# Optimization experiments

Measured on AMD Instinct MI355X. Metric: run time of the kernel, lower is better.

The kernel has to match this reference:

```python
import jax, jax.numpy as jnp
import numpy as np

N, E, D = 10000, 160000, 512


def setup_inputs() -> dict:
    key = jax.random.key(0)
    ks = jax.random.split(key, 5)
    x = jax.random.normal(ks[0], (N, D), dtype=jnp.float32)
    edge_index = jax.random.randint(ks[1], (2, E), 0, N, dtype=jnp.int32)
    W = jax.random.normal(ks[2], (D, D), dtype=jnp.float32) * (1.0 / np.sqrt(D))
    a_src = jax.random.normal(ks[3], (D,), dtype=jnp.float32) * 0.1
    a_dst = jax.random.normal(ks[4], (D,), dtype=jnp.float32) * 0.1
    bias = jnp.zeros((D,), dtype=jnp.float32)
    return {"x": x, "edge_index": edge_index, "W": W,
            "a_src": a_src, "a_dst": a_dst, "bias": bias}


def reference(x, edge_index, W, a_src, a_dst, bias):
    n = x.shape[0]
    # PyG GATConv default: add self-loops
    loops = jnp.arange(n, dtype=edge_index.dtype)
    src = jnp.concatenate([edge_index[0], loops])  # [E+N]
    dst = jnp.concatenate([edge_index[1], loops])  # [E+N]

    h = x @ W.T                                    # [N, D] linear projection
    e_src = h @ a_src                              # [N]
    e_dst = h @ a_dst                              # [N]
    e = e_src[src] + e_dst[dst]                    # [E+N]
    neg_slope = 0.2
    e = jnp.where(e > 0, e, neg_slope * e)         # leaky_relu

    # per-destination softmax (stable); self-loops guarantee non-empty segments
    m = jax.ops.segment_max(e, dst, num_segments=n)
    e = jnp.exp(e - m[dst])
    s = jax.ops.segment_sum(e, dst, num_segments=n)
    alpha = e / s[dst]                             # [E+N]

    msg = alpha[:, None] * h[src]                  # [E+N, D]
    out = jax.ops.segment_sum(msg, dst, num_segments=n) + bias  # [N, D]

    # module forward: x + elu(gat(x, edge_index))
    return x + jax.nn.elu(out)
```

## Files before the change

kernel.cpp:

```cpp
#include <hip/hip_runtime.h>
#include <hip/hip_bf16.h>

using bf16x8 = __attribute__((ext_vector_type(8))) __bf16;
using f32x4  = __attribute__((ext_vector_type(4))) float;
typedef unsigned int u32;

#define DFEAT 512
#define SLOTS 64

static __device__ __forceinline__ unsigned short f2bfbits(float f) {
    union { float f; unsigned int u; } v; v.f = f;
    unsigned int u = v.u;
    unsigned int r = (u + 0x7fffu + ((u >> 16) & 1u)) >> 16;
    return (unsigned short)r;
}

static __device__ __forceinline__ void gload16(const unsigned short* g, unsigned short* l) {
    __builtin_amdgcn_global_load_lds(
        (const __attribute__((address_space(1))) u32*)g,
        (__attribute__((address_space(3))) u32*)l, 16, 0, 0);
}

__global__ __launch_bounds__(256) void cvt_scatter_kernel(
    const float* __restrict__ x, const float* __restrict__ w,
    unsigned short* __restrict__ Xb, unsigned short* __restrict__ Wb,
    const int* __restrict__ srcv, const int* __restrict__ dstv,
    int* __restrict__ cur, int* __restrict__ slot,
    int nx4, int ntot4, int E, int T)
{
    int i = blockIdx.x * 256 + threadIdx.x;
    if (i < ntot4) {
        const float* in = (i < nx4) ? x : w;
        unsigned short* o = (i < nx4) ? Xb : Wb;
        int j = (i < nx4) ? i : i - nx4;
        float4 v = ((const float4*)in)[j];
        ushort4 u;
        u.x = f2bfbits(v.x); u.y = f2bfbits(v.y);
        u.z = f2bfbits(v.z); u.w = f2bfbits(v.w);
        ((ushort4*)o)[j] = u;
    }
    if (i < T) {
        int s, d;
        if (i < E) { s = srcv[i]; d = dstv[i]; }
        else       { s = d = i - E; }
        int pos = atomicAdd(&cur[d], 1);
        if (pos < SLOTS) slot[(size_t)d * SLOTS + pos] = s;
    }
}

__global__ __launch_bounds__(256, 5) void gemm_h_kernel(
    const unsigned short* __restrict__ X, const unsigned short* __restrict__ Wm,
    const float* __restrict__ avs, const float* __restrict__ avd,
    unsigned short* __restrict__ H, float* __restrict__ es, float* __restrict__ ed,
    int N)
{
    __shared__ unsigned short Asm[2][64 * 64];
    __shared__ unsigned short Bsm[2][64 * 64];

    int L = blockIdx.x;
    int xcd = L & 7;
    int q   = L >> 3;
    int rpan = (q >> 3) * 8 + xcd;
    int cpan = q & 7;
    int rowPanels = (N + 63) >> 6;
    if (rpan >= rowPanels) return;
    int bm = rpan * 64;
    int bn = cpan * 64;

    int tid  = threadIdx.x;
    int wave = tid >> 6;
    int lane = tid & 63;
    int l15  = lane & 15;
    int quad = lane >> 4;

    int srow   = lane >> 3;
    int schunk = (lane & 7) ^ (srow & 7);
    int arow0 = bm + wave * 16 + srow;
    int arow1 = arow0 + 8;
    arow0 = arow0 < N ? arow0 : N - 1;
    arow1 = arow1 < N ? arow1 : N - 1;
    const unsigned short* gA0 = X  + (size_t)arow0 * DFEAT + schunk * 8;
    const unsigned short* gA1 = X  + (size_t)arow1 * DFEAT + schunk * 8;
    const unsigned short* gB0 = Wm + (size_t)(bn + wave * 16 + srow) * DFEAT + schunk * 8;
    const unsigned short* gB1 = gB0 + (size_t)8 * DFEAT;

    auto stage = [&](int buf, int s) {
        int ko = s * 64;
        gload16(gA0 + ko, &Asm[buf][(wave * 16 + 0) * 64]);
        gload16(gA1 + ko, &Asm[buf][(wave * 16 + 8) * 64]);
        gload16(gB0 + ko, &Bsm[buf][(wave * 16 + 0) * 64]);
        gload16(gB1 + ko, &Bsm[buf][(wave * 16 + 8) * 64]);
    };

    f32x4 acc[4] = {};
    int xa = l15 & 7;
    int aoff = (wave * 16 + l15) * 128;

    auto compute = [&](int buf) {
        const char* Ab = (const char*)&Asm[buf][0];
        const char* Bb = (const char*)&Bsm[buf][0];
        #pragma unroll
        for (int ks = 0; ks < 2; ++ks) {
            int cb = ((ks * 4 + quad) ^ xa) * 16;
            bf16x8 a  = *(const bf16x8*)(Ab + aoff + cb);
            bf16x8 b0 = *(const bf16x8*)(Bb + (0 * 16 + l15) * 128 + cb);
            bf16x8 b1 = *(const bf16x8*)(Bb + (1 * 16 + l15) * 128 + cb);
            bf16x8 b2 = *(const bf16x8*)(Bb + (2 * 16 + l15) * 128 + cb);
            bf16x8 b3 = *(const bf16x8*)(Bb + (3 * 16 + l15) * 128 + cb);
            acc[0] = __builtin_amdgcn_mfma_f32_16x16x32_bf16(a, b0, acc[0], 0, 0, 0);
            acc[1] = __builtin_amdgcn_mfma_f32_16x16x32_bf16(a, b1, acc[1], 0, 0, 0);
            acc[2] = __builtin_amdgcn_mfma_f32_16x16x32_bf16(a, b2, acc[2], 0, 0, 0);
            acc[3] = __builtin_amdgcn_mfma_f32_16x16x32_bf16(a, b3, acc[3], 0, 0, 0);
        }
    };

    stage(0, 0);
    __syncthreads();
    int buf = 0;
    for (int s = 0; s < 7; ++s) {
        stage(buf ^ 1, s + 1);
        compute(buf);
        __syncthreads();
        buf ^= 1;
    }
    compute(buf);

    float as[4], ad[4];
    #pragma unroll
    for (int nt = 0; nt < 4; ++nt) {
        as[nt] = avs[bn + nt * 16 + l15];
        ad[nt] = avd[bn + nt * 16 + l15];
    }

    int rbase = bm + wave * 16 + quad * 4;
    #pragma unroll
    for (int nt = 0; nt < 4; ++nt) {
        int col = bn + nt * 16 + l15;
        #pragma unroll
        for (int r = 0; r < 4; ++r) {
            int row = rbase + r;
            if (row < N) H[(size_t)row * DFEAT + col] = f2bfbits(acc[nt][r]);
        }
    }
    #pragma unroll
    for (int r = 0; r < 4; ++r) {
        float ps = acc[0][r] * as[0] + acc[1][r] * as[1]
                 + acc[2][r] * as[2] + acc[3][r] * as[3];
        float pd = acc[0][r] * ad[0] + acc[1][r] * ad[1]
                 + acc[2][r] * ad[2] + acc[3][r] * ad[3];
        #pragma unroll
        for (int m = 1; m < 16; m <<= 1) {
            ps += __shfl_xor(ps, m);
            pd += __shfl_xor(pd, m);
        }
        int row = rbase + r;
        if (l15 == 0 && row < N) {
            atomicAdd(&es[row], ps);
            atomicAdd(&ed[row], pd);
        }
    }
}

__global__ __launch_bounds__(256) void aggregate_kernel(
    const unsigned short* __restrict__ H, const float* __restrict__ x,
    const float* __restrict__ bias,
    const int* __restrict__ cur, const int* __restrict__ slot,
    const float* __restrict__ es, const float* __restrict__ ed,
    float* __restrict__ out, int N)
{
    int node = (blockIdx.x * 256 + threadIdx.x) >> 6;
    int lane = threadIdx.x & 63;
    if (node >= N) return;

    int k = cur[node];
    if (k > SLOTS) k = SLOTS;

    int   s = 0;
    float w = 0.f;
    if (lane < k) {
        s = slot[(size_t)node * SLOTS + lane];
        float e = es[s] + ed[node];
        e = e > 0.f ? e : 0.2f * e;
        w = __expf(e);
    }
    float denom = w;
    #pragma unroll
    for (int off = 32; off > 0; off >>= 1) denom += __shfl_xor(denom, off);
    float inv = 1.0f / denom;

    float a[8] = {};
    const unsigned short* Hl = H + lane * 8;

    auto accum = [&](int sj, float wj) {
        uint4 hv = *(const uint4*)(Hl + (size_t)sj * DFEAT);
        a[0] += wj * __uint_as_float(hv.x << 16);
        a[1] += wj * __uint_as_float(hv.x & 0xffff0000u);
        a[2] += wj * __uint_as_float(hv.y << 16);
        a[3] += wj * __uint_as_float(hv.y & 0xffff0000u);
        a[4] += wj * __uint_as_float(hv.z << 16);
        a[5] += wj * __uint_as_float(hv.z & 0xffff0000u);
        a[6] += wj * __uint_as_float(hv.w << 16);
        a[7] += wj * __uint_as_float(hv.w & 0xffff0000u);
    };

    int j = 0;
    for (; j + 3 < k; j += 4) {
        int   s0 = __shfl(s, j),     s1 = __shfl(s, j + 1);
        int   s2 = __shfl(s, j + 2), s3 = __shfl(s, j + 3);
        float w0 = __shfl(w, j),     w1 = __shfl(w, j + 1);
        float w2 = __shfl(w, j + 2), w3 = __shfl(w, j + 3);
        uint4 h0 = *(const uint4*)(Hl + (size_t)s0 * DFEAT);
        uint4 h1 = *(const uint4*)(Hl + (size_t)s1 * DFEAT);
        uint4 h2 = *(const uint4*)(Hl + (size_t)s2 * DFEAT);
        uint4 h3 = *(const uint4*)(Hl + (size_t)s3 * DFEAT);
        a[0] += w0 * __uint_as_float(h0.x << 16);
        a[1] += w0 * __uint_as_float(h0.x & 0xffff0000u);
        a[2] += w0 * __uint_as_float(h0.y << 16);
        a[3] += w0 * __uint_as_float(h0.y & 0xffff0000u);
        a[4] += w0 * __uint_as_float(h0.z << 16);
        a[5] += w0 * __uint_as_float(h0.z & 0xffff0000u);
        a[6] += w0 * __uint_as_float(h0.w << 16);
        a[7] += w0 * __uint_as_float(h0.w & 0xffff0000u);
        a[0] += w1 * __uint_as_float(h1.x << 16);
        a[1] += w1 * __uint_as_float(h1.x & 0xffff0000u);
        a[2] += w1 * __uint_as_float(h1.y << 16);
        a[3] += w1 * __uint_as_float(h1.y & 0xffff0000u);
        a[4] += w1 * __uint_as_float(h1.z << 16);
        a[5] += w1 * __uint_as_float(h1.z & 0xffff0000u);
        a[6] += w1 * __uint_as_float(h1.w << 16);
        a[7] += w1 * __uint_as_float(h1.w & 0xffff0000u);
        a[0] += w2 * __uint_as_float(h2.x << 16);
        a[1] += w2 * __uint_as_float(h2.x & 0xffff0000u);
        a[2] += w2 * __uint_as_float(h2.y << 16);
        a[3] += w2 * __uint_as_float(h2.y & 0xffff0000u);
        a[4] += w2 * __uint_as_float(h2.z << 16);
        a[5] += w2 * __uint_as_float(h2.z & 0xffff0000u);
        a[6] += w2 * __uint_as_float(h2.w << 16);
        a[7] += w2 * __uint_as_float(h2.w & 0xffff0000u);
        a[0] += w3 * __uint_as_float(h3.x << 16);
        a[1] += w3 * __uint_as_float(h3.x & 0xffff0000u);
        a[2] += w3 * __uint_as_float(h3.y << 16);
        a[3] += w3 * __uint_as_float(h3.y & 0xffff0000u);
        a[4] += w3 * __uint_as_float(h3.z << 16);
        a[5] += w3 * __uint_as_float(h3.z & 0xffff0000u);
        a[6] += w3 * __uint_as_float(h3.w << 16);
        a[7] += w3 * __uint_as_float(h3.w & 0xffff0000u);
    }
    for (; j < k; ++j) accum(__shfl(s, j), __shfl(w, j));

    int c = lane * 8;
    float4 b0 = *(const float4*)(bias + c);
    float4 b1 = *(const float4*)(bias + c + 4);
    float4 x0 = *(const float4*)(x + (size_t)node * DFEAT + c);
    float4 x1 = *(const float4*)(x + (size_t)node * DFEAT + c + 4);
    float r[8];
    r[0] = a[0] * inv + b0.x; r[1] = a[1] * inv + b0.y;
    r[2] = a[2] * inv + b0.z; r[3] = a[3] * inv + b0.w;
    r[4] = a[4] * inv + b1.x; r[5] = a[5] * inv + b1.y;
    r[6] = a[6] * inv + b1.z; r[7] = a[7] * inv + b1.w;
    #pragma unroll
    for (int i = 0; i < 8; ++i)
        r[i] = r[i] > 0.f ? r[i] : __expf(r[i]) - 1.f;
    float4 o0 = make_float4(x0.x + r[0], x0.y + r[1], x0.z + r[2], x0.w + r[3]);
    float4 o1 = make_float4(x1.x + r[4], x1.y + r[5], x1.z + r[6], x1.w + r[7]);
    *(float4*)(out + (size_t)node * DFEAT + c)     = o0;
    *(float4*)(out + (size_t)node * DFEAT + c + 4) = o1;
}

extern "C" void kernel_launch(void* const* d_in, const int* in_sizes, int n_in,
                              void* d_out, int out_size, void* d_ws, size_t ws_size,
                              hipStream_t stream)
{
    const float* x    = (const float*)d_in[0];
    const int*   edge = (const int*)d_in[1];
    const float* Wm   = (const float*)d_in[2];
    const float* avs  = (const float*)d_in[3];
    const float* avd  = (const float*)d_in[4];
    const float* bias = (const float*)d_in[5];

    const int D = DFEAT;
    const int N = in_sizes[0] / D;
    const int E = in_sizes[1] / 2;
    const int T = E + N;
    const int* srcv = edge;
    const int* dstv = edge + E;

    char* ws = (char*)d_ws;
    size_t off = 0;
    auto alloc = [&](size_t bytes) -> char* {
        char* p = ws + off;
        off += (bytes + 255) & ~(size_t)255;
        return p;
    };
    int*   cur  = (int*)alloc((size_t)N * 3 * 4);
    float* es   = (float*)(cur + N);
    float* ed   = es + N;
    int*   slot = (int*)alloc((size_t)N * SLOTS * 4);
    unsigned short* Xb = (unsigned short*)alloc((size_t)N * D * 2);
    unsigned short* Wb = (unsigned short*)alloc((size_t)D * D * 2);
    unsigned short* H  = (unsigned short*)alloc((size_t)N * D * 2);

    hipMemsetAsync(cur, 0, (size_t)N * 3 * 4, stream);

    int nx4   = (N * D) / 4;
    int ntot4 = nx4 + (D * D) / 4;
    int grid0 = (ntot4 > T ? ntot4 : T);
    cvt_scatter_kernel<<<dim3((grid0 + 255) / 256), 256, 0, stream>>>(
        x, Wm, Xb, Wb, srcv, dstv, cur, slot, nx4, ntot4, E, T);

    int rowPanels  = (N + 63) / 64;
    int rowPanels8 = ((rowPanels + 7) / 8) * 8;
    gemm_h_kernel<<<dim3(rowPanels8 * 8), 256, 0, stream>>>(
        Xb, Wb, avs, avd, H, es, ed, N);
    aggregate_kernel<<<dim3((N * 64 + 255) / 256), 256, 0, stream>>>(
        H, x, bias, cur, slot, es, ed, (float*)d_out, N);
}
```

Baseline: 135.6 us.

## Enlarge GEMM row tile to 128 and unroll aggregation gathers by eight

The GEMM now computes a 128x64 tile per block, with each wave holding two 16-row sub-tiles. Each loaded B fragment is reused across two MFMAs, which roughly halves the number of blocks and the redundant loads of W. Occupancy is lowered to 3 blocks per SM to fit the larger accumulators and LDS. The aggregation loop issues eight independent row gathers per iteration instead of four, exposing more memory-level parallelism at the cost of more registers.

After: 132.9 us, median of 2. -2.0%, faster.

```diff
diff --git a/kernel.cpp b/kernel.cpp
--- a/kernel.cpp
+++ b/kernel.cpp
@@ -48,23 +48,23 @@
     }
 }
 
-__global__ __launch_bounds__(256, 5) void gemm_h_kernel(
+__global__ __launch_bounds__(256, 3) void gemm_h_kernel(
     const unsigned short* __restrict__ X, const unsigned short* __restrict__ Wm,
     const float* __restrict__ avs, const float* __restrict__ avd,
     unsigned short* __restrict__ H, float* __restrict__ es, float* __restrict__ ed,
     int N)
 {
-    __shared__ unsigned short Asm[2][64 * 64];
-    __shared__ unsigned short Bsm[2][64 * 64];
+    __shared__ __align__(16) unsigned short Asm[2][128 * 64];
+    __shared__ __align__(16) unsigned short Bsm[2][64 * 64];
 
     int L = blockIdx.x;
     int xcd = L & 7;
     int q   = L >> 3;
     int rpan = (q >> 3) * 8 + xcd;
     int cpan = q & 7;
-    int rowPanels = (N + 63) >> 6;
+    int rowPanels = (N + 127) >> 7;
     if (rpan >= rowPanels) return;
-    int bm = rpan * 64;
+    int bm = rpan * 128;
     int bn = cpan * 64;
 
     int tid  = threadIdx.x;
@@ -74,27 +74,38 @@
     int quad = lane >> 4;
 
     int srow   = lane >> 3;
-    int schunk = (lane & 7) ^ (srow & 7);
-    int arow0 = bm + wave * 16 + srow;
-    int arow1 = arow0 + 8;
-    arow0 = arow0 < N ? arow0 : N - 1;
-    arow1 = arow1 < N ? arow1 : N - 1;
-    const unsigned short* gA0 = X  + (size_t)arow0 * DFEAT + schunk * 8;
-    const unsigned short* gA1 = X  + (size_t)arow1 * DFEAT + schunk * 8;
+    int schunk = (lane & 7) ^ srow;
+    const unsigned short* gA0;
+    const unsigned short* gA1;
+    const unsigned short* gA2;
+    const unsigned short* gA3;
+    {
+        int r0 = bm + wave * 32 +  0 + srow; r0 = r0 < N ? r0 : N - 1;
+        int r1 = bm + wave * 32 +  8 + srow; r1 = r1 < N ? r1 : N - 1;
+        int r2 = bm + wave * 32 + 16 + srow; r2 = r2 < N ? r2 : N - 1;
+        int r3 = bm + wave * 32 + 24 + srow; r3 = r3 < N ? r3 : N - 1;
+        gA0 = X + (size_t)r0 * DFEAT + schunk * 8;
+        gA1 = X + (size_t)r1 * DFEAT + schunk * 8;
+        gA2 = X + (size_t)r2 * DFEAT + schunk * 8;
+        gA3 = X + (size_t)r3 * DFEAT + schunk * 8;
+    }
     const unsigned short* gB0 = Wm + (size_t)(bn + wave * 16 + srow) * DFEAT + schunk * 8;
     const unsigned short* gB1 = gB0 + (size_t)8 * DFEAT;
 
     auto stage = [&](int buf, int s) {
         int ko = s * 64;
-        gload16(gA0 + ko, &Asm[buf][(wave * 16 + 0) * 64]);
-        gload16(gA1 + ko, &Asm[buf][(wave * 16 + 8) * 64]);
+        gload16(gA0 + ko, &Asm[buf][(wave * 32 +  0) * 64]);
+        gload16(gA1 + ko, &Asm[buf][(wave * 32 +  8) * 64]);
+        gload16(gA2 + ko, &Asm[buf][(wave * 32 + 16) * 64]);
+        gload16(gA3 + ko, &Asm[buf][(wave * 32 + 24) * 64]);
         gload16(gB0 + ko, &Bsm[buf][(wave * 16 + 0) * 64]);
         gload16(gB1 + ko, &Bsm[buf][(wave * 16 + 8) * 64]);
     };
 
-    f32x4 acc[4] = {};
+    f32x4 acc[2][4] = {};
     int xa = l15 & 7;
-    int aoff = (wave * 16 + l15) * 128;
+    int aoff0 = (wave * 32 +  0 + l15) * 128;
+    int aoff1 = (wave * 32 + 16 + l15) * 128;
 
     auto compute = [&](int buf) {
         const char* Ab = (const char*)&Asm[buf][0];
@@ -102,15 +113,20 @@
         #pragma unroll
         for (int ks = 0; ks < 2; ++ks) {
             int cb = ((ks * 4 + quad) ^ xa) * 16;
-            bf16x8 a  = *(const bf16x8*)(Ab + aoff + cb);
+            bf16x8 a0 = *(const bf16x8*)(Ab + aoff0 + cb);
+            bf16x8 a1 = *(const bf16x8*)(Ab + aoff1 + cb);
             bf16x8 b0 = *(const bf16x8*)(Bb + (0 * 16 + l15) * 128 + cb);
             bf16x8 b1 = *(const bf16x8*)(Bb + (1 * 16 + l15) * 128 + cb);
             bf16x8 b2 = *(const bf16x8*)(Bb + (2 * 16 + l15) * 128 + cb);
             bf16x8 b3 = *(const bf16x8*)(Bb + (3 * 16 + l15) * 128 + cb);
-            acc[0] = __builtin_amdgcn_mfma_f32_16x16x32_bf16(a, b0, acc[0], 0, 0, 0);
-            acc[1] = __builtin_amdgcn_mfma_f32_16x16x32_bf16(a, b1, acc[1], 0, 0, 0);
-            acc[2] = __builtin_amdgcn_mfma_f32_16x16x32_bf16(a, b2, acc[2], 0, 0, 0);
-            acc[3] = __builtin_amdgcn_mfma_f32_16x16x32_bf16(a, b3, acc[3], 0, 0, 0);
+            acc[0][0] = __builtin_amdgcn_mfma_f32_16x16x32_bf16(a0, b0, acc[0][0], 0, 0, 0);
+            acc[1][0] = __builtin_amdgcn_mfma_f32_16x16x32_bf16(a1, b0, acc[1][0], 0, 0, 0);
+            acc[0][1] = __builtin_amdgcn_mfma_f32_16x16x32_bf16(a0, b1, acc[0][1], 0, 0, 0);
+            acc[1][1] = __builtin_amdgcn_mfma_f32_16x16x32_bf16(a1, b1, acc[1][1], 0, 0, 0);
+            acc[0][2] = __builtin_amdgcn_mfma_f32_16x16x32_bf16(a0, b2, acc[0][2], 0, 0, 0);
+            acc[1][2] = __builtin_amdgcn_mfma_f32_16x16x32_bf16(a1, b2, acc[1][2], 0, 0, 0);
+            acc[0][3] = __builtin_amdgcn_mfma_f32_16x16x32_bf16(a0, b3, acc[0][3], 0, 0, 0);
+            acc[1][3] = __builtin_amdgcn_mfma_f32_16x16x32_bf16(a1, b3, acc[1][3], 0, 0, 0);
         }
     };
 
@@ -132,31 +148,34 @@
         ad[nt] = avd[bn + nt * 16 + l15];
     }
 
-    int rbase = bm + wave * 16 + quad * 4;
     #pragma unroll
-    for (int nt = 0; nt < 4; ++nt) {
-        int col = bn + nt * 16 + l15;
+    for (int mt = 0; mt < 2; ++mt) {
+        int rbase = bm + wave * 32 + mt * 16 + quad * 4;
+        #pragma unroll
+        for (int nt = 0; nt < 4; ++nt) {
+            int col = bn + nt * 16 + l15;
+            #pragma unroll
+            for (int r = 0; r < 4; ++r) {
+                int row = rbase + r;
+                if (row < N) H[(size_t)row * DFEAT + col] = f2bfbits(acc[mt][nt][r]);
+            }
+        }
         #pragma unroll
         for (int r = 0; r < 4; ++r) {
+            float ps = acc[mt][0][r] * as[0] + acc[mt][1][r] * as[1]
+                     + acc[mt][2][r] * as[2] + acc[mt][3][r] * as[3];
+            float pd = acc[mt][0][r] * ad[0] + acc[mt][1][r] * ad[1]
+                     + acc[mt][2][r] * ad[2] + acc[mt][3][r] * ad[3];
+            #pragma unroll
+            for (int m = 1; m < 16; m <<= 1) {
+                ps += __shfl_xor(ps, m);
+                pd += __shfl_xor(pd, m);
+            }
             int row = rbase + r;
-            if (row < N) H[(size_t)row * DFEAT + col] = f2bfbits(acc[nt][r]);
-        }
-    }
-    #pragma unroll
-    for (int r = 0; r < 4; ++r) {
-        float ps = acc[0][r] * as[0] + acc[1][r] * as[1]
-                 + acc[2][r] * as[2] + acc[3][r] * as[3];
-        float pd = acc[0][r] * ad[0] + acc[1][r] * ad[1]
-                 + acc[2][r] * ad[2] + acc[3][r] * ad[3];
-        #pragma unroll
-        for (int m = 1; m < 16; m <<= 1) {
-            ps += __shfl_xor(ps, m);
-            pd += __shfl_xor(pd, m);
-        }
-        int row = rbase + r;
-        if (l15 == 0 && row < N) {
-            atomicAdd(&es[row], ps);
-            atomicAdd(&ed[row], pd);
+            if (l15 == 0 && row < N) {
+                atomicAdd(&es[row], ps);
+                atomicAdd(&ed[row], pd);
+            }
         }
     }
 }
@@ -191,8 +210,7 @@
     float a[8] = {};
     const unsigned short* Hl = H + lane * 8;
 
-    auto accum = [&](int sj, float wj) {
-        uint4 hv = *(const uint4*)(Hl + (size_t)sj * DFEAT);
+    auto fma8 = [&](uint4 hv, float wj) {
         a[0] += wj * __uint_as_float(hv.x << 16);
         a[1] += wj * __uint_as_float(hv.x & 0xffff0000u);
         a[2] += wj * __uint_as_float(hv.y << 16);
@@ -204,7 +222,27 @@
     };
 
     int j = 0;
-    for (; j + 3 < k; j += 4) {
+    for (; j + 7 < k; j += 8) {
+        int   s0 = __shfl(s, j),     s1 = __shfl(s, j + 1);
+        int   s2 = __shfl(s, j + 2), s3 = __shfl(s, j + 3);
+        int   s4 = __shfl(s, j + 4), s5 = __shfl(s, j + 5);
+        int   s6 = __shfl(s, j + 6), s7 = __shfl(s, j + 7);
+        float w0 = __shfl(w, j),     w1 = __shfl(w, j + 1);
+        float w2 = __shfl(w, j + 2), w3 = __shfl(w, j + 3);
+        float w4 = __shfl(w, j + 4), w5 = __shfl(w, j + 5);
+        float w6 = __shfl(w, j + 6), w7 = __shfl(w, j + 7);
+        uint4 h0 = *(const uint4*)(Hl + (size_t)s0 * DFEAT);
+        uint4 h1 = *(const uint4*)(Hl + (size_t)s1 * DFEAT);
+        uint4 h2 = *(const uint4*)(Hl + (size_t)s2 * DFEAT);
+        uint4 h3 = *(const uint4*)(Hl + (size_t)s3 * DFEAT);
+        uint4 h4 = *(const uint4*)(Hl + (size_t)s4 * DFEAT);
+        uint4 h5 = *(const uint4*)(Hl + (size_t)s5 * DFEAT);
+        uint4 h6 = *(const uint4*)(Hl + (size_t)s6 * DFEAT);
+        uint4 h7 = *(const uint4*)(Hl + (size_t)s7 * DFEAT);
+        fma8(h0, w0); fma8(h1, w1); fma8(h2, w2); fma8(h3, w3);
+        fma8(h4, w4); fma8(h5, w5); fma8(h6, w6); fma8(h7, w7);
+    }
+    if (j + 3 < k) {
         int   s0 = __shfl(s, j),     s1 = __shfl(s, j + 1);
         int   s2 = __shfl(s, j + 2), s3 = __shfl(s, j + 3);
         float w0 = __shfl(w, j),     w1 = __shfl(w, j + 1);
@@ -213,40 +251,13 @@
         uint4 h1 = *(const uint4*)(Hl + (size_t)s1 * DFEAT);
         uint4 h2 = *(const uint4*)(Hl + (size_t)s2 * DFEAT);
         uint4 h3 = *(const uint4*)(Hl + (size_t)s3 * DFEAT);
-        a[0] += w0 * __uint_as_float(h0.x << 16);
-        a[1] += w0 * __uint_as_float(h0.x & 0xffff0000u);
-        a[2] += w0 * __uint_as_float(h0.y << 16);
-        a[3] += w0 * __uint_as_float(h0.y & 0xffff0000u);
-        a[4] += w0 * __uint_as_float(h0.z << 16);
-        a[5] += w0 * __uint_as_float(h0.z & 0xffff0000u);
-        a[6] += w0 * __uint_as_float(h0.w << 16);
-        a[7] += w0 * __uint_as_float(h0.w & 0xffff0000u);
-        a[0] += w1 * __uint_as_float(h1.x << 16);
-        a[1] += w1 * __uint_as_float(h1.x & 0xffff0000u);
-        a[2] += w1 * __uint_as_float(h1.y << 16);
-        a[3] += w1 * __uint_as_float(h1.y & 0xffff0000u);
-        a[4] += w1 * __uint_as_float(h1.z << 16);
-        a[5] += w1 * __uint_as_float(h1.z & 0xffff0000u);
-        a[6] += w1 * __uint_as_float(h1.w << 16);
-        a[7] += w1 * __uint_as_float(h1.w & 0xffff0000u);
-        a[0] += w2 * __uint_as_float(h2.x << 16);
-        a[1] += w2 * __uint_as_float(h2.x & 0xffff0000u);
-        a[2] += w2 * __uint_as_float(h2.y << 16);
-        a[3] += w2 * __uint_as_float(h2.y & 0xffff0000u);
-        a[4] += w2 * __uint_as_float(h2.z << 16);
-        a[5] += w2 * __uint_as_float(h2.z & 0xffff0000u);
-        a[6] += w2 * __uint_as_float(h2.w << 16);
-        a[7] += w2 * __uint_as_float(h2.w & 0xffff0000u);
-        a[0] += w3 * __uint_as_float(h3.x << 16);
-        a[1] += w3 * __uint_as_float(h3.x & 0xffff0000u);
-        a[2] += w3 * __uint_as_float(h3.y << 16);
-        a[3] += w3 * __uint_as_float(h3.y & 0xffff0000u);
-        a[4] += w3 * __uint_as_float(h3.z << 16);
-        a[5] += w3 * __uint_as_float(h3.z & 0xffff0000u);
-        a[6] += w3 * __uint_as_float(h3.w << 16);
-        a[7] += w3 * __uint_as_float(h3.w & 0xffff0000u);
-    }
-    for (; j < k; ++j) accum(__shfl(s, j), __shfl(w, j));
+        fma8(h0, w0); fma8(h1, w1); fma8(h2, w2); fma8(h3, w3);
+        j += 4;
+    }
+    for (; j < k; ++j) {
+        uint4 hv = *(const uint4*)(Hl + (size_t)__shfl(s, j) * DFEAT);
+        fma8(hv, __shfl(w, j));
+    }
 
     int c = lane * 8;
     float4 b0 = *(const float4*)(bias + c);
@@ -308,7 +319,7 @@
     cvt_scatter_kernel<<<dim3((grid0 + 255) / 256), 256, 0, stream>>>(
         x, Wm, Xb, Wb, srcv, dstv, cur, slot, nx4, ntot4, E, T);
 
-    int rowPanels  = (N + 63) / 64;
+    int rowPanels  = (N + 127) / 128;
     int rowPanels8 = ((rowPanels + 7) / 8) * 8;
     gemm_h_kernel<<<dim3(rowPanels8 * 8), 256, 0, stream>>>(
         Xb, Wb, avs, avd, H, es, ed, N);
```
